# Performance work log

Measured on AMD Instinct MI355X. Metric: run time of the kernel, lower is better.

Reference implementation:

```python
import jax, jax.numpy as jnp
import numpy as np

N = 8192          # number of atoms
N_ELEM = 95       # r2r4 table size (elements 0..94)
EPS = 1e-12


def setup_inputs() -> dict:
    key = jax.random.key(0)
    k1, k2, k3 = jax.random.split(key, 3)
    atomic_numbers = jax.random.randint(k1, (N,), 0, N_ELEM)
    # positions in a ~60 Angstrom box so pair distances are realistic
    positions = jax.random.uniform(k2, (N, 3), dtype=jnp.float32) * 60.0
    r2r4 = jax.random.uniform(k3, (N_ELEM,), dtype=jnp.float32)
    # Becke-Johnson damping parameters (PBE D3-BJ)
    a1 = jnp.float32(0.4289)
    a2 = jnp.float32(4.4407)
    s6 = jnp.float32(1.0)
    s8 = jnp.float32(0.7875)
    return {"atomic_numbers": atomic_numbers, "positions": positions,
            "r2r4": r2r4, "a1": a1, "a2": a2, "s6": s6, "s8": s8}


def reference(atomic_numbers, positions, r2r4, a1, a2, s6, s8):
    # Per-atom-type gather (present in source; mathematically unused because
    # the source hard-codes c6 = c8 = 1 via all-ones LazyTensors).
    r2r4_z = r2r4[atomic_numbers]                      # (N,)

    # All-pairs squared distances. d appears only as d^6 and d^8, which are
    # polynomials in d2, so no sqrt is needed (also keeps diagonal smooth).
    diff = positions[:, None, :] - positions[None, :, :]   # (N, N, 3)
    d2 = jnp.sum(diff * diff, axis=-1)                     # (N, N)
    d6 = d2 * d2 * d2
    d8 = d6 * d2

    # c6 = c8 = 1  =>  tmp = a1 * sqrt(c8/c6) + a2 = a1 + a2
    tmp = a1 + a2
    tmp2 = tmp * tmp
    tmp6 = tmp2 * tmp2 * tmp2
    tmp8 = tmp6 * tmp2

    c6 = jnp.float32(1.0)
    c8 = jnp.float32(1.0)
    D_ij = -s6 * c6 / (d6 + tmp6 + EPS) - s8 * c8 / (d8 + tmp8 + EPS)

    # mask d > eps  <=>  d2 > eps^2 (removes self-terms)
    mask = d2 > EPS * EPS
    D_ij = jnp.where(mask, D_ij, jnp.float32(0.0))

    # a_i = sum_j D_ij ; energy = sum_i a_i
    return jnp.sum(D_ij) + jnp.float32(0.0) * jnp.sum(r2r4_z)
```

## Files before the change

kernel.cpp:

```cpp
#include <hip/hip_runtime.h>

#define NA 8192
#define IT 128
#define JT 64
#define NI (NA / IT)
#define NJOB 4160
#define WPB 8
#define BLOCK (WPB * 64)
#define NBLK (NJOB / WPB)
#define NSLOT 64
#define SLOT_STRIDE 16
#define NCH 4
#define S_OF(I) ((I) * (129 - (I)))

typedef float v2f __attribute__((ext_vector_type(2)));

__device__ __forceinline__ float bcast(float v, int k) {
    return __int_as_float(__builtin_amdgcn_readlane(__float_as_int(v), k));
}

__global__ __launch_bounds__(BLOCK, 4) void dftd3_pair_energy(
    const float* __restrict__ pos,
    const float* __restrict__ p_a1, const float* __restrict__ p_a2,
    const float* __restrict__ p_s6, const float* __restrict__ p_s8,
    float* __restrict__ slots, int* __restrict__ cnt,
    float* __restrict__ out)
{
    const int tid  = threadIdx.x;
    const int lane = tid & 63;
    const int w = __builtin_amdgcn_readfirstlane(blockIdx.x * WPB + (tid >> 6));

    int I = (int)((129.0f - sqrtf(16641.0f - 4.0f * (float)w)) * 0.5f);
    if (I < 0) I = 0;
    if (I > NI - 1) I = NI - 1;
    while (S_OF(I + 1) <= w) ++I;
    while (S_OF(I) > w) --I;
    const int J = 2 * I + (w - S_OF(I));
    const bool edge = (w - S_OF(I)) < 2;

    const float PS = 0.015625f;
    const int j = J * JT + lane;
    const float vxj = pos[3 * j + 0] * PS;
    const float vyj = pos[3 * j + 1] * PS;
    const float vzj = pos[3 * j + 2] * PS;

    const int i0 = I * IT + 2 * lane;
    const v2f xi = { pos[3 * i0 + 0] * PS, pos[3 * i0 + 3] * PS };
    const v2f yi = { pos[3 * i0 + 1] * PS, pos[3 * i0 + 4] * PS };
    const v2f zi = { pos[3 * i0 + 2] * PS, pos[3 * i0 + 5] * PS };

    const float a1 = p_a1[0], a2 = p_a2[0];
    const float s6 = p_s6[0], s8 = p_s8[0];
    const float tmp  = a1 + a2;
    const float tmp2 = tmp * tmp;
    const float tmp6 = tmp2 * tmp2 * tmp2;
    const float tmp8 = tmp6 * tmp2;
    const float T6s = (tmp6 + 1e-12f) * 1.4551915e-11f;
    const float T8s = (tmp8 + 1e-12f) * 3.5527137e-15f;
    const float c6 = -2.0f * s6 * 1.4551915e-11f;
    const float c8 = -2.0f * s8 * 3.5527137e-15f;

    v2f acc[NCH];
    #pragma unroll
    for (int c = 0; c < NCH; ++c) acc[c] = (v2f){0.0f, 0.0f};

    auto quad = [&](int k, bool masked) {
        v2f dx[NCH], dy[NCH], dz[NCH], d2[NCH], d4[NCH];
        v2f A[NCH], B[NCH], num[NCH], den[NCH];
        float r[NCH];
        #pragma unroll
        for (int c = 0; c < NCH; ++c) {
            const int kc = k + 16 * c;
            float sx = bcast(vxj, kc);
            float sy = bcast(vyj, kc);
            float sz = bcast(vzj, kc);
            dx[c] = xi - sx;
            dy[c] = yi - sy;
            dz[c] = zi - sz;
        }
        #pragma unroll
        for (int c = 0; c < NCH; ++c) {
            d2[c] = __builtin_elementwise_fma(dx[c], dx[c],
                    __builtin_elementwise_fma(dy[c], dy[c], dz[c] * dz[c]));
            d4[c] = d2[c] * d2[c];
        }
        #pragma unroll
        for (int c = 0; c < NCH; ++c) {
            A[c] = __builtin_elementwise_fma(d4[c], d2[c], (v2f)T6s);
            B[c] = __builtin_elementwise_fma(d4[c], d4[c], (v2f)T8s);
        }
        #pragma unroll
        for (int c = 0; c < NCH; ++c) {
            num[c] = __builtin_elementwise_fma((v2f)c6, B[c], (v2f)c8 * A[c]);
            den[c] = A[c] * B[c];
        }
        #pragma unroll
        for (int c = 0; c < NCH; ++c)
            r[c] = __builtin_amdgcn_rcpf(den[c].x * den[c].y);
        if (masked) {
            #pragma unroll
            for (int c = 0; c < NCH; ++c) {
                const int jk = J * JT + k + 16 * c;
                num[c].x = (jk > i0)     ? num[c].x : 0.0f;
                num[c].y = (jk > i0 + 1) ? num[c].y : 0.0f;
            }
        }
        #pragma unroll
        for (int c = 0; c < NCH; ++c) {
            v2f inv = { den[c].y * r[c], den[c].x * r[c] };
            acc[c] = __builtin_elementwise_fma(num[c], inv, acc[c]);
        }
    };

    if (edge) {
        #pragma unroll 2
        for (int k = 0; k < JT / NCH; ++k) quad(k, true);
    } else {
        #pragma unroll 2
        for (int k = 0; k < JT / NCH; ++k) quad(k, false);
    }

    v2f accv = (acc[0] + acc[1]) + (acc[2] + acc[3]);
    float acc_s = accv.x + accv.y;

    #pragma unroll
    for (int off = 32; off > 0; off >>= 1)
        acc_s += __shfl_xor(acc_s, off, 64);

    __shared__ float wsum[WPB];
    __shared__ int lastflag;
    if (lane == 0) wsum[tid >> 6] = acc_s;
    __syncthreads();
    if (tid == 0) {
        float s = 0.0f;
        #pragma unroll
        for (int q = 0; q < WPB; ++q) s += wsum[q];
        atomicAdd(&slots[(blockIdx.x & (NSLOT - 1)) * SLOT_STRIDE], s);
        __threadfence();
        int old = atomicAdd(cnt, 1);
        lastflag = (old == NBLK - 1);
    }
    __syncthreads();
    if (lastflag) {
        __threadfence();
        float s = 0.0f;
        if (tid < NSLOT)
            s = __hip_atomic_load(&slots[tid * SLOT_STRIDE],
                                  __ATOMIC_ACQUIRE, __HIP_MEMORY_SCOPE_AGENT);
        #pragma unroll
        for (int off = 32; off > 0; off >>= 1)
            s += __shfl_xor(s, off, 64);
        if (lane == 0) wsum[tid >> 6] = s;
        __syncthreads();
        if (tid == 0) out[0] = wsum[0];
    }
}

extern "C" void kernel_launch(void* const* d_in, const int* in_sizes, int n_in,
                              void* d_out, int out_size, void* d_ws, size_t ws_size,
                              hipStream_t stream) {
    const float* pos = (const float*)d_in[1];
    const float* a1  = (const float*)d_in[3];
    const float* a2  = (const float*)d_in[4];
    const float* s6  = (const float*)d_in[5];
    const float* s8  = (const float*)d_in[6];
    float* slots = (float*)d_ws;
    int*   cnt   = (int*)((char*)d_ws + NSLOT * SLOT_STRIDE * sizeof(float));
    float* out   = (float*)d_out;

    hipMemsetAsync(d_ws, 0, NSLOT * SLOT_STRIDE * sizeof(float) + sizeof(int), stream);

    dftd3_pair_energy<<<dim3(NBLK), BLOCK, 0, stream>>>(pos, a1, a2, s6, s8,
                                                        slots, cnt, out);
}
```

Before: 91.05 us.

## Compute pair distances via bf16 split MFMA dot products with norm expansion

```diff
diff --git a/kernel.cpp b/kernel.cpp
--- a/kernel.cpp
+++ b/kernel.cpp
@@ -1,26 +1,53 @@
 #include <hip/hip_runtime.h>
 
 #define NA 8192
-#define IT 128
-#define JT 64
-#define NI (NA / IT)
-#define NJOB 4160
 #define WPB 8
-#define BLOCK (WPB * 64)
+#define BLOCK 512
+#define NJOB 4224
 #define NBLK (NJOB / WPB)
 #define NSLOT 64
 #define SLOT_STRIDE 16
-#define NCH 4
-#define S_OF(I) ((I) * (129 - (I)))
+#define AB_OFF   0
+#define BB_OFF   262144
+#define SI_OFF   524288
+#define SLOT_OFF 557056
+#define CNT_OFF  561152
 
 typedef float v2f __attribute__((ext_vector_type(2)));
-
-__device__ __forceinline__ float bcast(float v, int k) {
-    return __int_as_float(__builtin_amdgcn_readlane(__float_as_int(v), k));
-}
-
-__global__ __launch_bounds__(BLOCK, 4) void dftd3_pair_energy(
-    const float* __restrict__ pos,
+typedef short short8 __attribute__((ext_vector_type(8)));
+typedef float f32x16 __attribute__((ext_vector_type(16)));
+
+__device__ __forceinline__ unsigned bf16rne(float f) {
+    unsigned u = __float_as_uint(f);
+    return (u + 0x7FFFu + ((u >> 16) & 1u)) >> 16;
+}
+
+__global__ __launch_bounds__(256) void prep(const float* __restrict__ pos,
+                                            uint4* __restrict__ Ab,
+                                            uint4* __restrict__ Bb,
+                                            float* __restrict__ Si)
+{
+    int a = blockIdx.x * 256 + threadIdx.x;
+    if (a >= NA) return;
+    const float PS = 0.015625f;
+    float x = pos[3*a+0] * PS, y = pos[3*a+1] * PS, z = pos[3*a+2] * PS;
+    unsigned xh = bf16rne(x); float fxh = __uint_as_float(xh << 16);
+    unsigned xl = bf16rne(x - fxh); float fxl = __uint_as_float(xl << 16);
+    unsigned yh = bf16rne(y); float fyh = __uint_as_float(yh << 16);
+    unsigned yl = bf16rne(y - fyh); float fyl = __uint_as_float(yl << 16);
+    unsigned zh = bf16rne(z); float fzh = __uint_as_float(zh << 16);
+    unsigned zl = bf16rne(z - fzh); float fzl = __uint_as_float(zl << 16);
+    float xe = fxh + fxl, ye = fyh + fyl, ze = fzh + fzl;
+    Si[a] = fmaf(xe, xe, fmaf(ye, ye, ze * ze));
+    Ab[2*a+0] = make_uint4(xh | (xh<<16), xl | (xl<<16), yh | (yh<<16), yl | (yl<<16));
+    Ab[2*a+1] = make_uint4(zh | (zh<<16), zl | (zl<<16), 0u, 0u);
+    Bb[2*a+0] = make_uint4(xh | (xl<<16), xh | (xl<<16), yh | (yl<<16), yh | (yl<<16));
+    Bb[2*a+1] = make_uint4(zh | (zl<<16), zh | (zl<<16), 0u, 0u);
+}
+
+__global__ __launch_bounds__(BLOCK, 4) void dftd3_mfma(
+    const uint4* __restrict__ Ab, const uint4* __restrict__ Bb,
+    const float* __restrict__ Si,
     const float* __restrict__ p_a1, const float* __restrict__ p_a2,
     const float* __restrict__ p_s6, const float* __restrict__ p_s8,
     float* __restrict__ slots, int* __restrict__ cnt,
@@ -30,24 +57,27 @@
     const int lane = tid & 63;
     const int w = __builtin_amdgcn_readfirstlane(blockIdx.x * WPB + (tid >> 6));
 
-    int I = (int)((129.0f - sqrtf(16641.0f - 4.0f * (float)w)) * 0.5f);
-    if (I < 0) I = 0;
-    if (I > NI - 1) I = NI - 1;
-    while (S_OF(I + 1) <= w) ++I;
-    while (S_OF(I) > w) --I;
-    const int J = 2 * I + (w - S_OF(I));
-    const bool edge = (w - S_OF(I)) < 2;
-
-    const float PS = 0.015625f;
-    const int j = J * JT + lane;
-    const float vxj = pos[3 * j + 0] * PS;
-    const float vyj = pos[3 * j + 1] * PS;
-    const float vzj = pos[3 * j + 2] * PS;
-
-    const int i0 = I * IT + 2 * lane;
-    const v2f xi = { pos[3 * i0 + 0] * PS, pos[3 * i0 + 3] * PS };
-    const v2f yi = { pos[3 * i0 + 1] * PS, pos[3 * i0 + 4] * PS };
-    const v2f zi = { pos[3 * i0 + 2] * PS, pos[3 * i0 + 5] * PS };
+    int q = (int)((260.0f - sqrtf(67600.0f - 16.0f * (float)w)) * 0.125f);
+    if (q < 0) q = 0;
+    if (q > 31) q = 31;
+    while (260*(q+1) - 4*(q+1)*(q+1) <= w) ++q;
+    while (260*q - 4*q*q > w) --q;
+    int r = w - (260*q - 4*q*q);
+    const int u = 32 - q;
+    int rowoff = 0;
+    while (r >= u) { r -= u; ++rowoff; }
+    const int I  = 8*q + rowoff;
+    const int Jc = q + r;
+
+    const int H = lane >> 5;
+    const int c = lane & 31;
+
+    const short8 af = __builtin_bit_cast(short8, Ab[(32*I + c)*2 + H]);
+
+    float4 siq[4];
+    const float4* Si4 = (const float4*)Si;
+    #pragma unroll
+    for (int g = 0; g < 4; ++g) siq[g] = Si4[8*I + 2*g + H];
 
     const float a1 = p_a1[0], a2 = p_a2[0];
     const float s6 = p_s6[0], s8 = p_s8[0];
@@ -57,71 +87,79 @@
     const float tmp8 = tmp6 * tmp2;
     const float T6s = (tmp6 + 1e-12f) * 1.4551915e-11f;
     const float T8s = (tmp8 + 1e-12f) * 3.5527137e-15f;
-    const float c6 = -2.0f * s6 * 1.4551915e-11f;
-    const float c8 = -2.0f * s8 * 3.5527137e-15f;
-
-    v2f acc[NCH];
-    #pragma unroll
-    for (int c = 0; c < NCH; ++c) acc[c] = (v2f){0.0f, 0.0f};
-
-    auto quad = [&](int k, bool masked) {
-        v2f dx[NCH], dy[NCH], dz[NCH], d2[NCH], d4[NCH];
-        v2f A[NCH], B[NCH], num[NCH], den[NCH];
-        float r[NCH];
-        #pragma unroll
-        for (int c = 0; c < NCH; ++c) {
-            const int kc = k + 16 * c;
-            float sx = bcast(vxj, kc);
-            float sy = bcast(vyj, kc);
-            float sz = bcast(vzj, kc);
-            dx[c] = xi - sx;
-            dy[c] = yi - sy;
-            dz[c] = zi - sz;
-        }
-        #pragma unroll
-        for (int c = 0; c < NCH; ++c) {
-            d2[c] = __builtin_elementwise_fma(dx[c], dx[c],
-                    __builtin_elementwise_fma(dy[c], dy[c], dz[c] * dz[c]));
-            d4[c] = d2[c] * d2[c];
-        }
-        #pragma unroll
-        for (int c = 0; c < NCH; ++c) {
-            A[c] = __builtin_elementwise_fma(d4[c], d2[c], (v2f)T6s);
-            B[c] = __builtin_elementwise_fma(d4[c], d4[c], (v2f)T8s);
-        }
-        #pragma unroll
-        for (int c = 0; c < NCH; ++c) {
-            num[c] = __builtin_elementwise_fma((v2f)c6, B[c], (v2f)c8 * A[c]);
-            den[c] = A[c] * B[c];
-        }
-        #pragma unroll
-        for (int c = 0; c < NCH; ++c)
-            r[c] = __builtin_amdgcn_rcpf(den[c].x * den[c].y);
-        if (masked) {
+    const float c6v = -s6 * 1.4551915e-11f;
+    const float c8v = -s8 * 3.5527137e-15f;
+
+    v2f aO = {0.0f, 0.0f};
+    v2f aD = {0.0f, 0.0f};
+
+    for (int t = 0; t < 8; ++t) {
+        const int J = 8*Jc + t;
+        if (J < I) continue;
+        const short8 bf_ = __builtin_bit_cast(short8, Bb[(32*J + c)*2 + H]);
+        const float Sj = Si[32*J + c];
+        f32x16 z = {};
+        f32x16 C = __builtin_amdgcn_mfma_f32_32x32x16_bf16(af, bf_, z, 0, 0, 0);
+
+        if (J > I) {
             #pragma unroll
-            for (int c = 0; c < NCH; ++c) {
-                const int jk = J * JT + k + 16 * c;
-                num[c].x = (jk > i0)     ? num[c].x : 0.0f;
-                num[c].y = (jk > i0 + 1) ? num[c].y : 0.0f;
+            for (int g = 0; g < 4; ++g) {
+                float4 s4 = siq[g];
+                v2f Sp01 = { s4.x + Sj, s4.y + Sj };
+                v2f Sp23 = { s4.z + Sj, s4.w + Sj };
+                v2f C01 = { C[4*g+0], C[4*g+1] };
+                v2f C23 = { C[4*g+2], C[4*g+3] };
+                v2f d2a = __builtin_elementwise_fma(C01, (v2f)(-2.0f), Sp01);
+                v2f d2b = __builtin_elementwise_fma(C23, (v2f)(-2.0f), Sp23);
+                v2f d4a = d2a * d2a,                  d4b = d2b * d2b;
+                v2f Aa = __builtin_elementwise_fma(d4a, d2a, (v2f)T6s);
+                v2f Ba = __builtin_elementwise_fma(d4a, d4a, (v2f)T8s);
+                v2f Ab_ = __builtin_elementwise_fma(d4b, d2b, (v2f)T6s);
+                v2f Bb_ = __builtin_elementwise_fma(d4b, d4b, (v2f)T8s);
+                v2f na = __builtin_elementwise_fma((v2f)c6v, Ba, (v2f)c8v * Aa);
+                v2f nb = __builtin_elementwise_fma((v2f)c6v, Bb_, (v2f)c8v * Ab_);
+                v2f da = Aa * Ba,                     db = Ab_ * Bb_;
+                float ra = __builtin_amdgcn_rcpf(da.x * da.y);
+                float rb = __builtin_amdgcn_rcpf(db.x * db.y);
+                v2f ia = { da.y * ra, da.x * ra };
+                v2f ib = { db.y * rb, db.x * rb };
+                aO = __builtin_elementwise_fma(na, ia, aO);
+                aO = __builtin_elementwise_fma(nb, ib, aO);
+            }
+        } else {
+            #pragma unroll
+            for (int g = 0; g < 4; ++g) {
+                const int base = 8*g + 4*H;
+                float4 s4 = siq[g];
+                v2f Sp01 = { s4.x + Sj, s4.y + Sj };
+                v2f Sp23 = { s4.z + Sj, s4.w + Sj };
+                v2f C01 = { C[4*g+0], C[4*g+1] };
+                v2f C23 = { C[4*g+2], C[4*g+3] };
+                v2f d2a = __builtin_elementwise_fma(C01, (v2f)(-2.0f), Sp01);
+                v2f d2b = __builtin_elementwise_fma(C23, (v2f)(-2.0f), Sp23);
+                v2f d4a = d2a * d2a,                  d4b = d2b * d2b;
+                v2f Aa = __builtin_elementwise_fma(d4a, d2a, (v2f)T6s);
+                v2f Ba = __builtin_elementwise_fma(d4a, d4a, (v2f)T8s);
+                v2f Ab_ = __builtin_elementwise_fma(d4b, d2b, (v2f)T6s);
+                v2f Bb_ = __builtin_elementwise_fma(d4b, d4b, (v2f)T8s);
+                v2f na = __builtin_elementwise_fma((v2f)c6v, Ba, (v2f)c8v * Aa);
+                v2f nb = __builtin_elementwise_fma((v2f)c6v, Bb_, (v2f)c8v * Ab_);
+                na.x = (c == base + 0) ? 0.0f : na.x;
+                na.y = (c == base + 1) ? 0.0f : na.y;
+                nb.x = (c == base + 2) ? 0.0f : nb.x;
+                nb.y = (c == base + 3) ? 0.0f : nb.y;
+                v2f da = Aa * Ba,                     db = Ab_ * Bb_;
+                float ra = __builtin_amdgcn_rcpf(da.x * da.y);
+                float rb = __builtin_amdgcn_rcpf(db.x * db.y);
+                v2f ia = { da.y * ra, da.x * ra };
+                v2f ib = { db.y * rb, db.x * rb };
+                aD = __builtin_elementwise_fma(na, ia, aD);
+                aD = __builtin_elementwise_fma(nb, ib, aD);
             }
         }
-        #pragma unroll
-        for (int c = 0; c < NCH; ++c) {
-            v2f inv = { den[c].y * r[c], den[c].x * r[c] };
-            acc[c] = __builtin_elementwise_fma(num[c], inv, acc[c]);
-        }
-    };
-
-    if (edge) {
-        #pragma unroll 2
-        for (int k = 0; k < JT / NCH; ++k) quad(k, true);
-    } else {
-        #pragma unroll 2
-        for (int k = 0; k < JT / NCH; ++k) quad(k, false);
     }
 
-    v2f accv = (acc[0] + acc[1]) + (acc[2] + acc[3]);
-    float acc_s = accv.x + accv.y;
+    float acc_s = 2.0f * (aO.x + aO.y) + (aD.x + aD.y);
 
     #pragma unroll
     for (int off = 32; off > 0; off >>= 1)
@@ -134,7 +172,7 @@
     if (tid == 0) {
         float s = 0.0f;
         #pragma unroll
-        for (int q = 0; q < WPB; ++q) s += wsum[q];
+        for (int k = 0; k < WPB; ++k) s += wsum[k];
         atomicAdd(&slots[(blockIdx.x & (NSLOT - 1)) * SLOT_STRIDE], s);
         __threadfence();
         int old = atomicAdd(cnt, 1);
@@ -164,12 +202,16 @@
     const float* a2  = (const float*)d_in[4];
     const float* s6  = (const float*)d_in[5];
     const float* s8  = (const float*)d_in[6];
-    float* slots = (float*)d_ws;
-    int*   cnt   = (int*)((char*)d_ws + NSLOT * SLOT_STRIDE * sizeof(float));
+    char* ws = (char*)d_ws;
+    uint4* Ab    = (uint4*)(ws + AB_OFF);
+    uint4* Bb    = (uint4*)(ws + BB_OFF);
+    float* Si    = (float*)(ws + SI_OFF);
+    float* slots = (float*)(ws + SLOT_OFF);
+    int*   cnt   = (int*)(ws + CNT_OFF);
     float* out   = (float*)d_out;
 
-    hipMemsetAsync(d_ws, 0, NSLOT * SLOT_STRIDE * sizeof(float) + sizeof(int), stream);
-
-    dftd3_pair_energy<<<dim3(NBLK), BLOCK, 0, stream>>>(pos, a1, a2, s6, s8,
-                                                        slots, cnt, out);
-}
+    prep<<<dim3(NA / 256), 256, 0, stream>>>(pos, Ab, Bb, Si);
+    hipMemsetAsync(ws + SLOT_OFF, 0, NSLOT * SLOT_STRIDE * sizeof(float) + sizeof(int), stream);
+    dftd3_mfma<<<dim3(NBLK), BLOCK, 0, stream>>>(Ab, Bb, Si, a1, a2, s6, s8,
+                                                 slots, cnt, out);
+}
```

After: 89.98 us. About the same (-1.2%).
